# Kernel tuning notes

Hardware: AMD Instinct MI355X
Metric: run time of the kernel (lower is better)

The kernel has to match this reference:

```python
import jax, jax.numpy as jnp
import numpy as np

TOP_K = 8
NUM_EXPERTS = 64
TEMPERATURE = 1.0
ALPHA = 0.01
EPS = 1e-20


def setup_inputs() -> dict:
    key = jax.random.key(0)
    k1, k2 = jax.random.split(key)
    hidden_states = jax.random.normal(k1, (4, 8192, 1024), dtype=jnp.float32)
    # kaiming_uniform-ish scale for the router weight
    bound = 1.0 / np.sqrt(1024.0)
    weight = jax.random.uniform(k2, (NUM_EXPERTS, 1024), dtype=jnp.float32,
                                minval=-bound, maxval=bound)
    return {"hidden_states": hidden_states, "weight": weight}


def reference(hidden_states, weight):
    bsz, seq_len, hidden_dim = hidden_states.shape
    flat = hidden_states.reshape(-1, hidden_dim)            # [N, H], N = bsz*seq_len
    logits = jnp.einsum('nh,eh->ne', flat, weight) / TEMPERATURE  # [N, E]
    scores = jax.nn.softmax(logits, axis=-1)                # [N, E]
    topk_weight, topk_idx = jax.lax.top_k(scores, TOP_K)    # [N, k] each
    # renormalize top-k probabilities
    topk_weight = topk_weight / (topk_weight.sum(axis=-1, keepdims=True) + EPS)
    # aux load-balancing loss (seq_aux=False branch), scores detached
    scores_aux = jax.lax.stop_gradient(scores)
    idx_flat = topk_idx.reshape(-1)                         # [N*k]
    ce = jnp.zeros((NUM_EXPERTS,), dtype=jnp.float32).at[idx_flat].add(1.0)
    ce = ce / idx_flat.shape[0]                             # mean of one-hot rows
    pi = scores_aux.mean(axis=0)                            # [E]
    fi = ce * NUM_EXPERTS
    aux_loss = (pi * fi).sum() * ALPHA
    return topk_idx, topk_weight, aux_loss
```

## Files before the change

### kernel.cpp

```cpp
#include <hip/hip_runtime.h>

#define H 1024
#define E 64
#define BT 64
#define THETA 2e-4f

typedef __attribute__((ext_vector_type(4))) float f4;
typedef __attribute__((ext_vector_type(16))) float f32x16;
typedef __bf16 bf16x8 __attribute__((ext_vector_type(8)));
typedef unsigned int u32;
typedef __attribute__((ext_vector_type(4))) u32 u32x4;

__device__ __forceinline__ u32 cvtpk_bf16(float a, float b) {
    u32 r;
    asm("v_cvt_pk_bf16_f32 %0, %1, %2" : "=v"(r) : "v"(a), "v"(b));
    return r;
}
__device__ __forceinline__ float asfloat(u32 u) { union { u32 u; float f; } c; c.u = u; return c.f; }

__device__ __forceinline__ void split8(f4 a, f4 b, u32x4& hi, u32x4& lo) {
    float x0[4] = {a.x, a.z, b.x, b.z};
    float x1[4] = {a.y, a.w, b.y, b.w};
    #pragma unroll
    for (int i = 0; i < 4; ++i) {
        u32 h = cvtpk_bf16(x0[i], x1[i]);
        float r0 = x0[i] - asfloat(h << 16);
        float r1 = x1[i] - asfloat(h & 0xFFFF0000u);
        hi[i] = h;
        lo[i] = cvtpk_bf16(r0, r1);
    }
}

__device__ __forceinline__ void async16(const void* g, void* l) {
    __builtin_amdgcn_global_load_lds(
        (const __attribute__((address_space(1))) unsigned int*)g,
        (__attribute__((address_space(3))) unsigned int*)l,
        16, 0, 0);
}

__global__ __launch_bounds__(512, 4)
void gate_main(const float* __restrict__ hs, const float* __restrict__ wt,
               float* __restrict__ out, float* __restrict__ pi_ws,
               float* __restrict__ ce_ws, unsigned int* __restrict__ risk_cnt,
               unsigned int* __restrict__ risk_list, unsigned int risk_cap,
               int n_tokens) {
    __shared__ float smem[16384];
    const int t = threadIdx.x;
    const int wave = t >> 6, lane = t & 63;
    const int tok_base = blockIdx.x * BT;
    char* sb = (char*)smem;

    const int srow = t >> 3;
    const int srcj = (t & 7) ^ (srow & 7);
    const float* gA = hs + (size_t)(tok_base + srow) * H + srcj * 4;
    const float* gB = wt + (size_t)srow * H + srcj * 4;
    const int sdest = wave << 10;

    const int lr = lane & 31, kh = lane >> 5;
    const int q4 = wave & 3, kh2 = wave >> 2;
    const int wrow = (q4 >> 1) * 32;
    const int wcol = (q4 & 1) * 32;
    const int arow = wrow + lr, brow = wcol + lr;
    const int s0 = kh2 * 4 + kh * 2;
    const int aoff = arow * 128 + ((s0 ^ (arow & 7)) << 4);
    const int boff = 8192 + brow * 128 + ((s0 ^ (brow & 7)) << 4);

    f32x16 acc0, acc1;
    #pragma unroll
    for (int i = 0; i < 16; ++i) { acc0[i] = 0.f; acc1[i] = 0.f; }

    auto stage = [&](int c) {
        char* bb = sb + (c & 3) * 16384;
        async16(gA + c * 32, bb + sdest);
        async16(gB + c * 32, bb + 8192 + sdest);
    };
    auto compute = [&](int c) {
        const char* cb = sb + (c & 3) * 16384;
        f4 a0 = *(const f4*)(cb + aoff);
        f4 a1 = *(const f4*)(cb + (aoff ^ 16));
        f4 b0 = *(const f4*)(cb + boff);
        f4 b1 = *(const f4*)(cb + (boff ^ 16));
        u32x4 ahp, alp, bhp, blp;
        split8(a0, a1, ahp, alp);
        split8(b0, b1, bhp, blp);
        const bf16x8 ah = __builtin_bit_cast(bf16x8, ahp);
        const bf16x8 al = __builtin_bit_cast(bf16x8, alp);
        const bf16x8 bh = __builtin_bit_cast(bf16x8, bhp);
        const bf16x8 bl = __builtin_bit_cast(bf16x8, blp);
        acc0 = __builtin_amdgcn_mfma_f32_32x32x16_bf16(ah, bh, acc0, 0, 0, 0);
        acc1 = __builtin_amdgcn_mfma_f32_32x32x16_bf16(ah, bl, acc1, 0, 0, 0);
        acc1 = __builtin_amdgcn_mfma_f32_32x32x16_bf16(al, bh, acc1, 0, 0, 0);
    };

    stage(0); stage(1); stage(2);
    for (int c = 0; c < 30; ++c) {
        asm volatile("s_waitcnt vmcnt(4)" ::: "memory");
        __builtin_amdgcn_s_barrier();
        __builtin_amdgcn_sched_barrier(0);
        if (c < 29) stage(c + 3);
        __builtin_amdgcn_sched_barrier(0);
        compute(c);
    }
    asm volatile("s_waitcnt vmcnt(2)" ::: "memory");
    __builtin_amdgcn_s_barrier();
    __builtin_amdgcn_sched_barrier(0);
    compute(30);
    asm volatile("s_waitcnt vmcnt(0)" ::: "memory");
    __builtin_amdgcn_s_barrier();
    __builtin_amdgcn_sched_barrier(0);
    compute(31);
    __syncthreads();

    float* S = smem;
    f4* S4 = (f4*)smem;
    float* P2    = smem + 4352;
    float* recip = smem + 8448;
    float* hist  = smem + 8512;
    float* pi7   = smem + 8576;

    {
        float vs[16];
        #pragma unroll
        for (int i = 0; i < 16; ++i) vs[i] = acc0[i] + acc1[i];
        if (kh2) {
            #pragma unroll
            for (int gq = 0; gq < 4; ++gq)
                #pragma unroll
                for (int qq = 0; qq < 4; ++qq)
                    P2[q4 * 1024 + (qq + gq * 8 + kh * 4) * 32 + lr] = vs[gq * 4 + qq];
        }
        if (t < 64) hist[t] = 0.f;
        __syncthreads();
        if (!kh2) {
            #pragma unroll
            for (int gq = 0; gq < 4; ++gq)
                #pragma unroll
                for (int qq = 0; qq < 4; ++qq) {
                    const int row = qq + gq * 8 + kh * 4;
                    S[(wrow + row) * 68 + wcol + lr] =
                        vs[gq * 4 + qq] + P2[q4 * 1024 + row * 32 + lr];
                }
        }
    }
    __syncthreads();

    if (t < 256) {
        const int tok = t >> 2, q = t & 3;
        f4 v[4];
        #pragma unroll
        for (int c2 = 0; c2 < 4; ++c2) v[c2] = S4[tok * 17 + q * 4 + c2];
        float m = v[0].x;
        #pragma unroll
        for (int c2 = 0; c2 < 4; ++c2)
            m = fmaxf(m, fmaxf(fmaxf(v[c2].x, v[c2].y), fmaxf(v[c2].z, v[c2].w)));
        m = fmaxf(m, __shfl_xor(m, 1, 64));
        m = fmaxf(m, __shfl_xor(m, 2, 64));
        float lsum = 0.f;
        #pragma unroll
        for (int c2 = 0; c2 < 4; ++c2) {
            v[c2].x = __expf(v[c2].x - m); v[c2].y = __expf(v[c2].y - m);
            v[c2].z = __expf(v[c2].z - m); v[c2].w = __expf(v[c2].w - m);
            lsum += (v[c2].x + v[c2].y) + (v[c2].z + v[c2].w);
        }
        #pragma unroll
        for (int c2 = 0; c2 < 4; ++c2) S4[tok * 17 + q * 4 + c2] = v[c2];
        lsum += __shfl_xor(lsum, 1, 64);
        lsum += __shfl_xor(lsum, 2, 64);
        if (q == 0) recip[tok] = 1.0f / lsum;
    }
    __syncthreads();

    const int selw = blockIdx.x & 7;
    if (wave == selw) {
        const int tok = lane;
        const int tok_g = tok_base + tok;
        float val[9]; int idx[9];
        #pragma unroll
        for (int r = 0; r < 9; ++r) { val[r] = -1.f; idx[r] = 0; }
        #pragma unroll
        for (int c2 = 0; c2 < 16; ++c2) {
            f4 v = S4[tok * 17 + c2];
            float e4[4] = {v.x, v.y, v.z, v.w};
            #pragma unroll
            for (int u = 0; u < 4; ++u) {
                float cv = e4[u]; int ci = c2 * 4 + u;
                #pragma unroll
                for (int r = 0; r < 9; ++r) {
                    const bool g = cv > val[r];
                    const float tv = val[r]; const int ti = idx[r];
                    val[r] = g ? cv : tv;  idx[r] = g ? ci : ti;
                    cv = g ? tv : cv;      ci = g ? ti : ci;
                }
            }
        }
        const float s8 = ((val[0] + val[1]) + (val[2] + val[3]))
                       + ((val[4] + val[5]) + (val[6] + val[7]));
        const float wsum = s8 + 1e-20f;
        f4* out4 = (f4*)out;
        f4 o;
        o.x = (float)idx[0]; o.y = (float)idx[1]; o.z = (float)idx[2]; o.w = (float)idx[3];
        out4[(size_t)tok_g * 2] = o;
        o.x = (float)idx[4]; o.y = (float)idx[5]; o.z = (float)idx[6]; o.w = (float)idx[7];
        out4[(size_t)tok_g * 2 + 1] = o;
        const size_t wb = (size_t)n_tokens * 2;
        o.x = val[0] / wsum; o.y = val[1] / wsum; o.z = val[2] / wsum; o.w = val[3] / wsum;
        out4[wb + (size_t)tok_g * 2] = o;
        o.x = val[4] / wsum; o.y = val[5] / wsum; o.z = val[6] / wsum; o.w = val[7] / wsum;
        out4[wb + (size_t)tok_g * 2 + 1] = o;
        #pragma unroll
        for (int r = 0; r < 8; ++r) atomicAdd(&hist[idx[r]], 1.0f);
        float ming = 1e30f;
        #pragma unroll
        for (int r = 0; r < 8; ++r)
            ming = fminf(ming, (val[r] - val[r + 1]) / fmaxf(val[r], 1e-30f));
        if (ming < THETA) {
            unsigned int pos = atomicAdd(risk_cnt, 1u);
            if (pos < risk_cap) risk_list[pos] = (unsigned int)tok_g;
        }
    } else {
        const int sev = ((wave - selw) & 7) - 1;
        const int e = lane;
        const int t0 = sev * 9;
        const int t1 = (sev == 6) ? 64 : (t0 + 9);
        float part = 0.f;
        for (int tok = t0; tok < t1; ++tok)
            part = fmaf(S[tok * 68 + e], recip[tok], part);
        pi7[sev * 64 + e] = part;
    }
    __syncthreads();
    const int rep = (blockIdx.x & 7) << 6;
    if (t < 64) {
        const float p = ((pi7[t] + pi7[64 + t]) + (pi7[128 + t] + pi7[192 + t]))
                      + ((pi7[256 + t] + pi7[320 + t]) + pi7[384 + t]);
        atomicAdd(&pi_ws[rep + t], p);
    } else if (t < 128) {
        atomicAdd(&ce_ws[rep + (t - 64)], hist[t - 64]);
    }
}

__global__ __launch_bounds__(256)
void gate_fixup(const float* __restrict__ hs, const float* __restrict__ wt,
                float* __restrict__ out, const unsigned int* __restrict__ risk_cnt,
                const unsigned int* __restrict__ risk_list, unsigned int risk_cap,
                int n_tokens, const float* __restrict__ pi_ws,
                const float* __restrict__ ce_ws) {
    __shared__ float hrow[H];
    __shared__ double red[256];
    const int t = threadIdx.x;

    if (blockIdx.x == 0 && t < 64) {
        double pi = 0.0, ce = 0.0;
        #pragma unroll
        for (int rp = 0; rp < 8; ++rp) {
            pi += (double)pi_ws[rp * 64 + t];
            ce += (double)ce_ws[rp * 64 + t];
        }
        pi /= (double)n_tokens;
        ce /= ((double)n_tokens * 8.0);
        double term = pi * ce * 64.0;
        #pragma unroll
        for (int off = 32; off > 0; off >>= 1) term += __shfl_xor(term, off, 64);
        if (t == 0) out[(size_t)n_tokens * 16] = (float)(term * 0.01);
    }

    unsigned int cnt = *risk_cnt;
    if (cnt > risk_cap) cnt = risk_cap;

    for (unsigned int u = blockIdx.x; u < cnt; u += gridDim.x) {
        const int tok = (int)risk_list[u];
        ((float4*)hrow)[t] = ((const float4*)(hs + (size_t)tok * H))[t];
        __syncthreads();

        const int e = t >> 2, sl = t & 3;
        const float4* wp = (const float4*)wt + (size_t)e * 256;
        const float4* hp = (const float4*)hrow;
        double acc = 0.0;
        #pragma unroll 8
        for (int k4 = 0; k4 < 64; ++k4) {
            float4 wv = wp[k4 * 4 + sl];
            float4 hv = hp[k4 * 4 + sl];
            acc = fma((double)wv.x, (double)hv.x, acc);
            acc = fma((double)wv.y, (double)hv.y, acc);
            acc = fma((double)wv.z, (double)hv.z, acc);
            acc = fma((double)wv.w, (double)hv.w, acc);
        }
        red[t] = acc;
        __syncthreads();

        if (t < 64) {
            const int lane = t;
            double lg = red[t * 4] + red[t * 4 + 1] + red[t * 4 + 2] + red[t * 4 + 3];
            double m = lg;
            #pragma unroll
            for (int off = 32; off > 0; off >>= 1) {
                double o = __shfl_xor(m, off, 64);
                m = (o > m) ? o : m;
            }
            const double p = exp(lg - m);
            double v = lg, psum = 0.0, mypv = 0.0;
            int myidx = 0;
            for (int r = 0; r < 8; ++r) {
                double bv = v; int bi = lane;
                #pragma unroll
                for (int off = 32; off > 0; off >>= 1) {
                    double ov = __shfl_xor(bv, off, 64);
                    int    oi = __shfl_xor(bi, off, 64);
                    if (ov > bv || (ov == bv && oi < bi)) { bv = ov; bi = oi; }
                }
                double pw = __shfl(p, bi, 64);
                psum += pw;
                if (lane == r) { myidx = bi; mypv = pw; }
                if (lane == bi) v = -1e300;
            }
            const double wsum = psum + 1e-20;
            if (lane < 8) {
                out[(size_t)tok * 8 + lane] = (float)myidx;
                out[(size_t)n_tokens * 8 + (size_t)tok * 8 + lane] = (float)(mypv / wsum);
            }
        }
        __syncthreads();
    }
}

extern "C" void kernel_launch(void* const* d_in, const int* in_sizes, int n_in,
                              void* d_out, int out_size, void* d_ws, size_t ws_size,
                              hipStream_t stream) {
    const float* hs = (const float*)d_in[0];
    const float* wt = (const float*)d_in[1];
    float* out = (float*)d_out;
    const int n_tokens = in_sizes[0] / H;

    float* pi_ws = (float*)d_ws;
    float* ce_ws = (float*)((char*)d_ws + 2048);
    unsigned int* risk_cnt  = (unsigned int*)((char*)d_ws + 4096);
    unsigned int* risk_list = (unsigned int*)((char*)d_ws + 4608);
    unsigned int risk_cap = (unsigned int)((ws_size > 4608 ? (ws_size - 4608) : 0) / 4);
    if (risk_cap > (unsigned int)n_tokens) risk_cap = (unsigned int)n_tokens;

    size_t zbytes = ws_size < 4608 ? ws_size : 4608;
    hipMemsetAsync(d_ws, 0, zbytes, stream);

    gate_main<<<n_tokens / BT, 512, 0, stream>>>(hs, wt, out, pi_ws, ce_ws,
                                                 risk_cnt, risk_list, risk_cap, n_tokens);
    gate_fixup<<<256, 256, 0, stream>>>(hs, wt, out, risk_cnt, risk_list, risk_cap,
                                        n_tokens, pi_ws, ce_ws);
}
```

Measured before the change: 238.5 us.

## Halve token tile to 32 with 256-thread blocks, 3-stage ring and fragment prefetch

```diff
diff --git a/kernel.cpp b/kernel.cpp
--- a/kernel.cpp
+++ b/kernel.cpp
@@ -2,8 +2,8 @@
 
 #define H 1024
 #define E 64
-#define BT 64
-#define THETA 2e-4f
+#define BT 32
+#define THETA 1e-4f
 
 typedef __attribute__((ext_vector_type(4))) float f4;
 typedef __attribute__((ext_vector_type(16))) float f32x16;
@@ -38,85 +38,99 @@
         16, 0, 0);
 }
 
-__global__ __launch_bounds__(512, 4)
+__global__ __launch_bounds__(256, 4)
 void gate_main(const float* __restrict__ hs, const float* __restrict__ wt,
                float* __restrict__ out, float* __restrict__ pi_ws,
                float* __restrict__ ce_ws, unsigned int* __restrict__ risk_cnt,
                unsigned int* __restrict__ risk_list, unsigned int risk_cap,
                int n_tokens) {
-    __shared__ float smem[16384];
+    __shared__ float smem[9216];
     const int t = threadIdx.x;
     const int wave = t >> 6, lane = t & 63;
     const int tok_base = blockIdx.x * BT;
     char* sb = (char*)smem;
 
-    const int srow = t >> 3;
-    const int srcj = (t & 7) ^ (srow & 7);
-    const float* gA = hs + (size_t)(tok_base + srow) * H + srcj * 4;
-    const float* gB = wt + (size_t)srow * H + srcj * 4;
-    const int sdest = wave << 10;
+    const int arow_s  = t >> 3;
+    const int aslot_s = (t & 7) ^ (arow_s & 7);
+    const float* gA  = hs + (size_t)(tok_base + arow_s) * H + aslot_s * 4;
+    const int brow1  = t >> 3;
+    const int bslot1 = (t & 7) ^ (brow1 & 7);
+    const float* gB1 = wt + (size_t)brow1 * H + bslot1 * 4;
+    const int brow2  = (t + 256) >> 3;
+    const int bslot2 = (t & 7) ^ (brow2 & 7);
+    const float* gB2 = wt + (size_t)brow2 * H + bslot2 * 4;
+    const int dA  = t * 16;
+    const int dB1 = 4096 + t * 16;
+    const int dB2 = 8192 + t * 16;
 
     const int lr = lane & 31, kh = lane >> 5;
-    const int q4 = wave & 3, kh2 = wave >> 2;
-    const int wrow = (q4 >> 1) * 32;
-    const int wcol = (q4 & 1) * 32;
-    const int arow = wrow + lr, brow = wcol + lr;
+    const int e2 = wave & 1, kh2 = wave >> 1;
     const int s0 = kh2 * 4 + kh * 2;
-    const int aoff = arow * 128 + ((s0 ^ (arow & 7)) << 4);
-    const int boff = 8192 + brow * 128 + ((s0 ^ (brow & 7)) << 4);
+    const int arow = lr;
+    const int brow = e2 * 32 + lr;
+    const int aoff0 = arow * 128 + ((s0 ^ (arow & 7)) << 4);
+    const int aoff1 = arow * 128 + (((s0 + 1) ^ (arow & 7)) << 4);
+    const int boff0 = 4096 + brow * 128 + ((s0 ^ (brow & 7)) << 4);
+    const int boff1 = 4096 + brow * 128 + (((s0 + 1) ^ (brow & 7)) << 4);
 
     f32x16 acc0, acc1;
     #pragma unroll
     for (int i = 0; i < 16; ++i) { acc0[i] = 0.f; acc1[i] = 0.f; }
 
     auto stage = [&](int c) {
-        char* bb = sb + (c & 3) * 16384;
-        async16(gA + c * 32, bb + sdest);
-        async16(gB + c * 32, bb + 8192 + sdest);
+        char* bb = sb + (c % 3) * 12288;
+        const int co = c * 32;
+        async16(gA  + co, bb + dA);
+        async16(gB1 + co, bb + dB1);
+        async16(gB2 + co, bb + dB2);
     };
-    auto compute = [&](int c) {
-        const char* cb = sb + (c & 3) * 16384;
-        f4 a0 = *(const f4*)(cb + aoff);
-        f4 a1 = *(const f4*)(cb + (aoff ^ 16));
-        f4 b0 = *(const f4*)(cb + boff);
-        f4 b1 = *(const f4*)(cb + (boff ^ 16));
+
+    f4 fa0[2], fa1[2], fb0[2], fb1[2];
+    auto fragread = [&](int c, int p) {
+        const char* cb = sb + (c % 3) * 12288;
+        fa0[p] = *(const f4*)(cb + aoff0);
+        fa1[p] = *(const f4*)(cb + aoff1);
+        fb0[p] = *(const f4*)(cb + boff0);
+        fb1[p] = *(const f4*)(cb + boff1);
+    };
+    auto computeF = [&](int p) {
         u32x4 ahp, alp, bhp, blp;
-        split8(a0, a1, ahp, alp);
-        split8(b0, b1, bhp, blp);
+        split8(fa0[p], fa1[p], ahp, alp);
+        split8(fb0[p], fb1[p], bhp, blp);
         const bf16x8 ah = __builtin_bit_cast(bf16x8, ahp);
         const bf16x8 al = __builtin_bit_cast(bf16x8, alp);
         const bf16x8 bh = __builtin_bit_cast(bf16x8, bhp);
         const bf16x8 bl = __builtin_bit_cast(bf16x8, blp);
+        __builtin_amdgcn_s_setprio(1);
         acc0 = __builtin_amdgcn_mfma_f32_32x32x16_bf16(ah, bh, acc0, 0, 0, 0);
         acc1 = __builtin_amdgcn_mfma_f32_32x32x16_bf16(ah, bl, acc1, 0, 0, 0);
         acc1 = __builtin_amdgcn_mfma_f32_32x32x16_bf16(al, bh, acc1, 0, 0, 0);
+        __builtin_amdgcn_s_setprio(0);
     };
 
-    stage(0); stage(1); stage(2);
-    for (int c = 0; c < 30; ++c) {
-        asm volatile("s_waitcnt vmcnt(4)" ::: "memory");
-        __builtin_amdgcn_s_barrier();
-        __builtin_amdgcn_sched_barrier(0);
-        if (c < 29) stage(c + 3);
-        __builtin_amdgcn_sched_barrier(0);
-        compute(c);
-    }
-    asm volatile("s_waitcnt vmcnt(2)" ::: "memory");
+    stage(0); stage(1);
+    asm volatile("s_waitcnt vmcnt(3)" ::: "memory");
     __builtin_amdgcn_s_barrier();
-    __builtin_amdgcn_sched_barrier(0);
-    compute(30);
-    asm volatile("s_waitcnt vmcnt(0)" ::: "memory");
-    __builtin_amdgcn_s_barrier();
-    __builtin_amdgcn_sched_barrier(0);
-    compute(31);
+    fragread(0, 0);
+    #pragma unroll 2
+    for (int c = 0; c < 32; ++c) {
+        if (c + 2 < 32) stage(c + 2);
+        if (c + 1 < 32) {
+            if (c + 1 < 31) { asm volatile("s_waitcnt vmcnt(3)" ::: "memory"); }
+            else            { asm volatile("s_waitcnt vmcnt(0)" ::: "memory"); }
+            __builtin_amdgcn_s_barrier();
+            fragread(c + 1, (c + 1) & 1);
+        }
+        computeF(c & 1);
+    }
     __syncthreads();
 
     float* S = smem;
     f4* S4 = (f4*)smem;
-    float* P2    = smem + 4352;
-    float* recip = smem + 8448;
-    float* hist  = smem + 8512;
-    float* pi7   = smem + 8576;
+    float* P2    = smem + 2176;
+    float* recip = smem + 4224;
+    float* hist  = smem + 4256;
+    float* pi3   = smem + 4320;
 
     {
         float vs[16];
@@ -127,7 +141,7 @@
             for (int gq = 0; gq < 4; ++gq)
                 #pragma unroll
                 for (int qq = 0; qq < 4; ++qq)
-                    P2[q4 * 1024 + (qq + gq * 8 + kh * 4) * 32 + lr] = vs[gq * 4 + qq];
+                    P2[e2 * 1024 + (qq + gq * 8 + kh * 4) * 32 + lr] = vs[gq * 4 + qq];
         }
         if (t < 64) hist[t] = 0.f;
         __syncthreads();
@@ -137,14 +151,14 @@
                 #pragma unroll
                 for (int qq = 0; qq < 4; ++qq) {
                     const int row = qq + gq * 8 + kh * 4;
-                    S[(wrow + row) * 68 + wcol + lr] =
-                        vs[gq * 4 + qq] + P2[q4 * 1024 + row * 32 + lr];
+                    S[row * 68 + e2 * 32 + lr] =
+                        vs[gq * 4 + qq] + P2[e2 * 1024 + row * 32 + lr];
                 }
         }
     }
     __syncthreads();
 
-    if (t < 256) {
+    if (t < 128) {
         const int tok = t >> 2, q = t & 3;
         f4 v[4];
         #pragma unroll
@@ -170,69 +184,69 @@
     }
     __syncthreads();
 
-    const int selw = blockIdx.x & 7;
+    const int selw = blockIdx.x & 3;
     if (wave == selw) {
-        const int tok = lane;
-        const int tok_g = tok_base + tok;
-        float val[9]; int idx[9];
-        #pragma unroll
-        for (int r = 0; r < 9; ++r) { val[r] = -1.f; idx[r] = 0; }
-        #pragma unroll
-        for (int c2 = 0; c2 < 16; ++c2) {
-            f4 v = S4[tok * 17 + c2];
-            float e4[4] = {v.x, v.y, v.z, v.w};
-            #pragma unroll
-            for (int u = 0; u < 4; ++u) {
-                float cv = e4[u]; int ci = c2 * 4 + u;
+        if (lane < 32) {
+            const int tok = lane;
+            const int tok_g = tok_base + tok;
+            float val[9]; int idx[9];
+            #pragma unroll
+            for (int r = 0; r < 9; ++r) { val[r] = -1.f; idx[r] = 0; }
+            #pragma unroll
+            for (int c2 = 0; c2 < 16; ++c2) {
+                f4 v = S4[tok * 17 + c2];
+                float e4[4] = {v.x, v.y, v.z, v.w};
                 #pragma unroll
-                for (int r = 0; r < 9; ++r) {
-                    const bool g = cv > val[r];
-                    const float tv = val[r]; const int ti = idx[r];
-                    val[r] = g ? cv : tv;  idx[r] = g ? ci : ti;
-                    cv = g ? tv : cv;      ci = g ? ti : ci;
+                for (int u = 0; u < 4; ++u) {
+                    float cv = e4[u]; int ci = c2 * 4 + u;
+                    #pragma unroll
+                    for (int r = 0; r < 9; ++r) {
+                        const bool g = cv > val[r];
+                        const float tv = val[r]; const int ti = idx[r];
+                        val[r] = g ? cv : tv;  idx[r] = g ? ci : ti;
+                        cv = g ? tv : cv;      ci = g ? ti : ci;
+                    }
                 }
             }
-        }
-        const float s8 = ((val[0] + val[1]) + (val[2] + val[3]))
-                       + ((val[4] + val[5]) + (val[6] + val[7]));
-        const float wsum = s8 + 1e-20f;
-        f4* out4 = (f4*)out;
-        f4 o;
-        o.x = (float)idx[0]; o.y = (float)idx[1]; o.z = (float)idx[2]; o.w = (float)idx[3];
-        out4[(size_t)tok_g * 2] = o;
-        o.x = (float)idx[4]; o.y = (float)idx[5]; o.z = (float)idx[6]; o.w = (float)idx[7];
-        out4[(size_t)tok_g * 2 + 1] = o;
-        const size_t wb = (size_t)n_tokens * 2;
-        o.x = val[0] / wsum; o.y = val[1] / wsum; o.z = val[2] / wsum; o.w = val[3] / wsum;
-        out4[wb + (size_t)tok_g * 2] = o;
-        o.x = val[4] / wsum; o.y = val[5] / wsum; o.z = val[6] / wsum; o.w = val[7] / wsum;
-        out4[wb + (size_t)tok_g * 2 + 1] = o;
-        #pragma unroll
-        for (int r = 0; r < 8; ++r) atomicAdd(&hist[idx[r]], 1.0f);
-        float ming = 1e30f;
-        #pragma unroll
-        for (int r = 0; r < 8; ++r)
-            ming = fminf(ming, (val[r] - val[r + 1]) / fmaxf(val[r], 1e-30f));
-        if (ming < THETA) {
-            unsigned int pos = atomicAdd(risk_cnt, 1u);
-            if (pos < risk_cap) risk_list[pos] = (unsigned int)tok_g;
+            const float s8 = ((val[0] + val[1]) + (val[2] + val[3]))
+                           + ((val[4] + val[5]) + (val[6] + val[7]));
+            const float wsum = s8 + 1e-20f;
+            f4* out4 = (f4*)out;
+            f4 o;
+            o.x = (float)idx[0]; o.y = (float)idx[1]; o.z = (float)idx[2]; o.w = (float)idx[3];
+            out4[(size_t)tok_g * 2] = o;
+            o.x = (float)idx[4]; o.y = (float)idx[5]; o.z = (float)idx[6]; o.w = (float)idx[7];
+            out4[(size_t)tok_g * 2 + 1] = o;
+            const size_t wb = (size_t)n_tokens * 2;
+            o.x = val[0] / wsum; o.y = val[1] / wsum; o.z = val[2] / wsum; o.w = val[3] / wsum;
+            out4[wb + (size_t)tok_g * 2] = o;
+            o.x = val[4] / wsum; o.y = val[5] / wsum; o.z = val[6] / wsum; o.w = val[7] / wsum;
+            out4[wb + (size_t)tok_g * 2 + 1] = o;
+            #pragma unroll
+            for (int r = 0; r < 8; ++r) atomicAdd(&hist[idx[r]], 1.0f);
+            float ming = 1e30f;
+            #pragma unroll
+            for (int r = 0; r < 8; ++r)
+                ming = fminf(ming, (val[r] - val[r + 1]) / fmaxf(val[r], 1e-30f));
+            if (ming < THETA) {
+                unsigned int pos = atomicAdd(risk_cnt, 1u);
+                if (pos < risk_cap) risk_list[pos] = (unsigned int)tok_g;
+            }
         }
     } else {
-        const int sev = ((wave - selw) & 7) - 1;
+        const int third = ((wave - selw) & 3) - 1;
         const int e = lane;
-        const int t0 = sev * 9;
-        const int t1 = (sev == 6) ? 64 : (t0 + 9);
+        const int t0 = third * 11;
+        const int t1 = (third == 2) ? 32 : (t0 + 11);
         float part = 0.f;
         for (int tok = t0; tok < t1; ++tok)
             part = fmaf(S[tok * 68 + e], recip[tok], part);
-        pi7[sev * 64 + e] = part;
+        pi3[third * 64 + e] = part;
     }
     __syncthreads();
     const int rep = (blockIdx.x & 7) << 6;
     if (t < 64) {
-        const float p = ((pi7[t] + pi7[64 + t]) + (pi7[128 + t] + pi7[192 + t]))
-                      + ((pi7[256 + t] + pi7[320 + t]) + pi7[384 + t]);
-        atomicAdd(&pi_ws[rep + t], p);
+        atomicAdd(&pi_ws[rep + t], pi3[t] + pi3[64 + t] + pi3[128 + t]);
     } else if (t < 128) {
         atomicAdd(&ce_ws[rep + (t - 64)], hist[t - 64]);
     }
@@ -340,7 +354,7 @@
     size_t zbytes = ws_size < 4608 ? ws_size : 4608;
     hipMemsetAsync(d_ws, 0, zbytes, stream);
 
-    gate_main<<<n_tokens / BT, 512, 0, stream>>>(hs, wt, out, pi_ws, ce_ws,
+    gate_main<<<n_tokens / BT, 256, 0, stream>>>(hs, wt, out, pi_ws, ce_ws,
                                                  risk_cnt, risk_list, risk_cap, n_tokens);
     gate_fixup<<<256, 256, 0, stream>>>(hs, wt, out, risk_cnt, risk_list, risk_cap,
                                         n_tokens, pi_ws, ce_ws);
```

New measurement: 237.4 us. No clear change (-0.5%).

## Double token tile to 128 with 1024 threads, load router weights directly to registers

Applied to the files above, without the earlier changes.

```diff
diff --git a/kernel.cpp b/kernel.cpp
--- a/kernel.cpp
+++ b/kernel.cpp
@@ -2,8 +2,8 @@
 
 #define H 1024
 #define E 64
-#define BT 64
-#define THETA 2e-4f
+#define BT 128
+#define THETA 1e-4f
 
 typedef __attribute__((ext_vector_type(4))) float f4;
 typedef __attribute__((ext_vector_type(16))) float f32x16;
@@ -38,13 +38,13 @@
         16, 0, 0);
 }
 
-__global__ __launch_bounds__(512, 4)
+__global__ __launch_bounds__(1024, 4)
 void gate_main(const float* __restrict__ hs, const float* __restrict__ wt,
                float* __restrict__ out, float* __restrict__ pi_ws,
                float* __restrict__ ce_ws, unsigned int* __restrict__ risk_cnt,
                unsigned int* __restrict__ risk_list, unsigned int risk_cap,
                int n_tokens) {
-    __shared__ float smem[16384];
+    __shared__ float smem[12288];
     const int t = threadIdx.x;
     const int wave = t >> 6, lane = t & 63;
     const int tok_base = blockIdx.x * BT;
@@ -53,36 +53,53 @@
     const int srow = t >> 3;
     const int srcj = (t & 7) ^ (srow & 7);
     const float* gA = hs + (size_t)(tok_base + srow) * H + srcj * 4;
-    const float* gB = wt + (size_t)srow * H + srcj * 4;
     const int sdest = wave << 10;
 
     const int lr = lane & 31, kh = lane >> 5;
-    const int q4 = wave & 3, kh2 = wave >> 2;
-    const int wrow = (q4 >> 1) * 32;
-    const int wcol = (q4 & 1) * 32;
-    const int arow = wrow + lr, brow = wcol + lr;
+    const int tq = wave & 3, ch = (wave >> 2) & 1, kh2 = wave >> 3;
+    const int wrow = tq * 32, wcol = ch * 32;
+    const int arow = wrow + lr;
     const int s0 = kh2 * 4 + kh * 2;
-    const int aoff = arow * 128 + ((s0 ^ (arow & 7)) << 4);
-    const int boff = 8192 + brow * 128 + ((s0 ^ (brow & 7)) << 4);
+    const int aoff0 = arow * 128 + (((s0    ) ^ (arow & 7)) << 4);
+    const int aoff1 = arow * 128 + (((s0 + 1) ^ (arow & 7)) << 4);
+    const float* gB = wt + (size_t)(wcol + lr) * H + kh2 * 16 + kh * 8;
 
     f32x16 acc0, acc1;
     #pragma unroll
     for (int i = 0; i < 16; ++i) { acc0[i] = 0.f; acc1[i] = 0.f; }
 
     auto stage = [&](int c) {
-        char* bb = sb + (c & 3) * 16384;
+        char* bb = sb + (c % 3) * 16384;
         async16(gA + c * 32, bb + sdest);
-        async16(gB + c * 32, bb + 8192 + sdest);
     };
-    auto compute = [&](int c) {
-        const char* cb = sb + (c & 3) * 16384;
-        f4 a0 = *(const f4*)(cb + aoff);
-        f4 a1 = *(const f4*)(cb + (aoff ^ 16));
-        f4 b0 = *(const f4*)(cb + boff);
-        f4 b1 = *(const f4*)(cb + (boff ^ 16));
+
+    f4 b0a, b1a, b0b, b1b;
+
+    stage(0); stage(1);
+    b0a = *(const f4*)(gB);
+    b1a = *(const f4*)(gB + 4);
+
+    #pragma unroll 2
+    for (int c = 0; c < 32; ++c) {
+        __builtin_amdgcn_sched_barrier(0);
+        if (c < 31) { asm volatile("s_waitcnt vmcnt(3)" ::: "memory"); }
+        else        { asm volatile("s_waitcnt vmcnt(2)" ::: "memory"); }
+        __builtin_amdgcn_s_barrier();
+        __builtin_amdgcn_sched_barrier(0);
+        if (c + 1 < 32) {
+            const float* p = gB + (c + 1) * 32;
+            if ((c & 1) == 0) { b0b = *(const f4*)p; b1b = *(const f4*)(p + 4); }
+            else              { b0a = *(const f4*)p; b1a = *(const f4*)(p + 4); }
+        }
+        if (c + 2 < 32) stage(c + 2);
+        __builtin_amdgcn_sched_barrier(0);
+        const char* cb = sb + (c % 3) * 16384;
+        f4 a0 = *(const f4*)(cb + aoff0);
+        f4 a1 = *(const f4*)(cb + aoff1);
         u32x4 ahp, alp, bhp, blp;
         split8(a0, a1, ahp, alp);
-        split8(b0, b1, bhp, blp);
+        if ((c & 1) == 0) split8(b0a, b1a, bhp, blp);
+        else              split8(b0b, b1b, bhp, blp);
         const bf16x8 ah = __builtin_bit_cast(bf16x8, ahp);
         const bf16x8 al = __builtin_bit_cast(bf16x8, alp);
         const bf16x8 bh = __builtin_bit_cast(bf16x8, bhp);
@@ -90,61 +107,43 @@
         acc0 = __builtin_amdgcn_mfma_f32_32x32x16_bf16(ah, bh, acc0, 0, 0, 0);
         acc1 = __builtin_amdgcn_mfma_f32_32x32x16_bf16(ah, bl, acc1, 0, 0, 0);
         acc1 = __builtin_amdgcn_mfma_f32_32x32x16_bf16(al, bh, acc1, 0, 0, 0);
-    };
-
-    stage(0); stage(1); stage(2);
-    for (int c = 0; c < 30; ++c) {
-        asm volatile("s_waitcnt vmcnt(4)" ::: "memory");
-        __builtin_amdgcn_s_barrier();
-        __builtin_amdgcn_sched_barrier(0);
-        if (c < 29) stage(c + 3);
-        __builtin_amdgcn_sched_barrier(0);
-        compute(c);
-    }
-    asm volatile("s_waitcnt vmcnt(2)" ::: "memory");
-    __builtin_amdgcn_s_barrier();
-    __builtin_amdgcn_sched_barrier(0);
-    compute(30);
-    asm volatile("s_waitcnt vmcnt(0)" ::: "memory");
-    __builtin_amdgcn_s_barrier();
-    __builtin_amdgcn_sched_barrier(0);
-    compute(31);
+    }
     __syncthreads();
 
     float* S = smem;
     f4* S4 = (f4*)smem;
-    float* P2    = smem + 4352;
-    float* recip = smem + 8448;
-    float* hist  = smem + 8512;
-    float* pi7   = smem + 8576;
+    float* recip = smem + 8704;
+    float* hist  = smem + 8832;
+    float* pi14  = smem + 8896;
 
     {
         float vs[16];
         #pragma unroll
         for (int i = 0; i < 16; ++i) vs[i] = acc0[i] + acc1[i];
-        if (kh2) {
-            #pragma unroll
-            for (int gq = 0; gq < 4; ++gq)
-                #pragma unroll
-                for (int qq = 0; qq < 4; ++qq)
-                    P2[q4 * 1024 + (qq + gq * 8 + kh * 4) * 32 + lr] = vs[gq * 4 + qq];
-        }
-        if (t < 64) hist[t] = 0.f;
-        __syncthreads();
         if (!kh2) {
             #pragma unroll
             for (int gq = 0; gq < 4; ++gq)
                 #pragma unroll
                 for (int qq = 0; qq < 4; ++qq) {
                     const int row = qq + gq * 8 + kh * 4;
-                    S[(wrow + row) * 68 + wcol + lr] =
-                        vs[gq * 4 + qq] + P2[q4 * 1024 + row * 32 + lr];
+                    S[(wrow + row) * 68 + wcol + lr] = vs[gq * 4 + qq];
                 }
         }
+        if (t < 64) hist[t] = 0.f;
+        __syncthreads();
+        if (kh2) {
+            #pragma unroll
+            for (int gq = 0; gq < 4; ++gq)
+                #pragma unroll
+                for (int qq = 0; qq < 4; ++qq) {
+                    const int row = qq + gq * 8 + kh * 4;
+                    atomicAdd(&S[(wrow + row) * 68 + wcol + lr], vs[gq * 4 + qq]);
+                }
+        }
     }
     __syncthreads();
 
-    if (t < 256) {
+    if (t < 512) {
         const int tok = t >> 2, q = t & 3;
         f4 v[4];
         #pragma unroll
@@ -170,9 +169,8 @@
     }
     __syncthreads();
 
-    const int selw = blockIdx.x & 7;
-    if (wave == selw) {
-        const int tok = lane;
+    if (wave >= 14) {
+        const int tok = (wave - 14) * 64 + lane;
         const int tok_g = tok_base + tok;
         float val[9]; int idx[9];
         #pragma unroll
@@ -218,20 +216,20 @@
             if (pos < risk_cap) risk_list[pos] = (unsigned int)tok_g;
         }
     } else {
-        const int sev = ((wave - selw) & 7) - 1;
         const int e = lane;
-        const int t0 = sev * 9;
-        const int t1 = (sev == 6) ? 64 : (t0 + 9);
+        const int t0 = (wave * 128) / 14;
+        const int t1 = ((wave + 1) * 128) / 14;
         float part = 0.f;
         for (int tok = t0; tok < t1; ++tok)
             part = fmaf(S[tok * 68 + e], recip[tok], part);
-        pi7[sev * 64 + e] = part;
+        pi14[wave * 64 + e] = part;
     }
     __syncthreads();
     const int rep = (blockIdx.x & 7) << 6;
     if (t < 64) {
-        const float p = ((pi7[t] + pi7[64 + t]) + (pi7[128 + t] + pi7[192 + t]))
-                      + ((pi7[256 + t] + pi7[320 + t]) + pi7[384 + t]);
+        float p = 0.f;
+        #pragma unroll
+        for (int i = 0; i < 14; ++i) p += pi14[i * 64 + t];
         atomicAdd(&pi_ws[rep + t], p);
     } else if (t < 128) {
         atomicAdd(&ce_ws[rep + (t - 64)], hist[t - 64]);
@@ -340,8 +338,8 @@
     size_t zbytes = ws_size < 4608 ? ws_size : 4608;
     hipMemsetAsync(d_ws, 0, zbytes, stream);
 
-    gate_main<<<n_tokens / BT, 512, 0, stream>>>(hs, wt, out, pi_ws, ce_ws,
-                                                 risk_cnt, risk_list, risk_cap, n_tokens);
+    gate_main<<<n_tokens / BT, 1024, 0, stream>>>(hs, wt, out, pi_ws, ce_ws,
+                                                  risk_cnt, risk_list, risk_cap, n_tokens);
     gate_fixup<<<256, 256, 0, stream>>>(hs, wt, out, risk_cnt, risk_list, risk_cap,
                                         n_tokens, pi_ws, ce_ws);
 }
```

New measurement: 251.6 us. 1.05x slower.

## Load router weights directly into registers and halve LDS staging buffers

Applied to the files above, without the earlier changes.

```diff
diff --git a/kernel.cpp b/kernel.cpp
--- a/kernel.cpp
+++ b/kernel.cpp
@@ -3,7 +3,7 @@
 #define H 1024
 #define E 64
 #define BT 64
-#define THETA 2e-4f
+#define THETA 1e-4f
 
 typedef __attribute__((ext_vector_type(4))) float f4;
 typedef __attribute__((ext_vector_type(16))) float f32x16;
@@ -44,7 +44,7 @@
                float* __restrict__ ce_ws, unsigned int* __restrict__ risk_cnt,
                unsigned int* __restrict__ risk_list, unsigned int risk_cap,
                int n_tokens) {
-    __shared__ float smem[16384];
+    __shared__ float smem[8192];
     const int t = threadIdx.x;
     const int wave = t >> 6, lane = t & 63;
     const int tok_base = blockIdx.x * BT;
@@ -53,36 +53,33 @@
     const int srow = t >> 3;
     const int srcj = (t & 7) ^ (srow & 7);
     const float* gA = hs + (size_t)(tok_base + srow) * H + srcj * 4;
-    const float* gB = wt + (size_t)srow * H + srcj * 4;
     const int sdest = wave << 10;
 
     const int lr = lane & 31, kh = lane >> 5;
     const int q4 = wave & 3, kh2 = wave >> 2;
     const int wrow = (q4 >> 1) * 32;
     const int wcol = (q4 & 1) * 32;
-    const int arow = wrow + lr, brow = wcol + lr;
+    const int arow = wrow + lr;
     const int s0 = kh2 * 4 + kh * 2;
-    const int aoff = arow * 128 + ((s0 ^ (arow & 7)) << 4);
-    const int boff = 8192 + brow * 128 + ((s0 ^ (brow & 7)) << 4);
+    const int aoff0 = arow * 128 + (((s0    ) ^ (arow & 7)) << 4);
+    const int aoff1 = arow * 128 + (((s0 + 1) ^ (arow & 7)) << 4);
+    const float* gBb = wt + (size_t)(wcol + lr) * H + s0 * 4;
 
     f32x16 acc0, acc1;
     #pragma unroll
     for (int i = 0; i < 16; ++i) { acc0[i] = 0.f; acc1[i] = 0.f; }
 
     auto stage = [&](int c) {
-        char* bb = sb + (c & 3) * 16384;
+        char* bb = sb + (c & 3) * 8192;
         async16(gA + c * 32, bb + sdest);
-        async16(gB + c * 32, bb + 8192 + sdest);
     };
-    auto compute = [&](int c) {
-        const char* cb = sb + (c & 3) * 16384;
-        f4 a0 = *(const f4*)(cb + aoff);
-        f4 a1 = *(const f4*)(cb + (aoff ^ 16));
-        f4 b0 = *(const f4*)(cb + boff);
-        f4 b1 = *(const f4*)(cb + (boff ^ 16));
+    auto compute = [&](int c, f4 bb0, f4 bb1) {
+        const char* cb = sb + (c & 3) * 8192;
+        f4 a0 = *(const f4*)(cb + aoff0);
+        f4 a1 = *(const f4*)(cb + aoff1);
         u32x4 ahp, alp, bhp, blp;
         split8(a0, a1, ahp, alp);
-        split8(b0, b1, bhp, blp);
+        split8(bb0, bb1, bhp, blp);
         const bf16x8 ah = __builtin_bit_cast(bf16x8, ahp);
         const bf16x8 al = __builtin_bit_cast(bf16x8, alp);
         const bf16x8 bh = __builtin_bit_cast(bf16x8, bhp);
@@ -92,53 +89,82 @@
         acc1 = __builtin_amdgcn_mfma_f32_32x32x16_bf16(al, bh, acc1, 0, 0, 0);
     };
 
+    f4 b0a = *(const f4*)(gBb);
+    f4 b1a = *(const f4*)(gBb + 4);
+    f4 b0b, b1b;
     stage(0); stage(1); stage(2);
-    for (int c = 0; c < 30; ++c) {
-        asm volatile("s_waitcnt vmcnt(4)" ::: "memory");
+
+    asm volatile("s_waitcnt vmcnt(2)" ::: "memory");
+    __builtin_amdgcn_s_barrier();
+    __builtin_amdgcn_sched_barrier(0);
+    b0b = *(const f4*)(gBb + 32); b1b = *(const f4*)(gBb + 36);
+    stage(3);
+    __builtin_amdgcn_sched_barrier(0);
+    compute(0, b0a, b1a);
+
+    asm volatile("s_waitcnt vmcnt(4)" ::: "memory");
+    __builtin_amdgcn_s_barrier();
+    __builtin_amdgcn_sched_barrier(0);
+    b0a = *(const f4*)(gBb + 64); b1a = *(const f4*)(gBb + 68);
+    stage(4);
+    __builtin_amdgcn_sched_barrier(0);
+    compute(1, b0b, b1b);
+
+    #pragma unroll 2
+    for (int c = 2; c < 30; ++c) {
+        asm volatile("s_waitcnt vmcnt(6)" ::: "memory");
         __builtin_amdgcn_s_barrier();
         __builtin_amdgcn_sched_barrier(0);
+        const float* p = gBb + (c + 1) * 32;
+        if ((c & 1) == 0) { b0b = *(const f4*)p; b1b = *(const f4*)(p + 4); }
+        else              { b0a = *(const f4*)p; b1a = *(const f4*)(p + 4); }
         if (c < 29) stage(c + 3);
         __builtin_amdgcn_sched_barrier(0);
-        compute(c);
-    }
-    asm volatile("s_waitcnt vmcnt(2)" ::: "memory");
+        if ((c & 1) == 0) compute(c, b0a, b1a);
+        else              compute(c, b0b, b1b);
+    }
+
+    asm volatile("s_waitcnt vmcnt(5)" ::: "memory");
     __builtin_amdgcn_s_barrier();
     __builtin_amdgcn_sched_barrier(0);
-    compute(30);
-    asm volatile("s_waitcnt vmcnt(0)" ::: "memory");
+    b0b = *(const f4*)(gBb + 31 * 32); b1b = *(const f4*)(gBb + 31 * 32 + 4);
+    __builtin_amdgcn_sched_barrier(0);
+    compute(30, b0a, b1a);
+
+    asm volatile("s_waitcnt vmcnt(4)" ::: "memory");
     __builtin_amdgcn_s_barrier();
     __builtin_amdgcn_sched_barrier(0);
-    compute(31);
+    compute(31, b0b, b1b);
     __syncthreads();
 
     float* S = smem;
     f4* S4 = (f4*)smem;
-    float* P2    = smem + 4352;
-    float* recip = smem + 8448;
-    float* hist  = smem + 8512;
-    float* pi7   = smem + 8576;
+    float* recip = smem + 4352;
+    float* hist  = smem + 4416;
+    float* pi7   = smem + 4480;
 
     {
         float vs[16];
         #pragma unroll
         for (int i = 0; i < 16; ++i) vs[i] = acc0[i] + acc1[i];
-        if (kh2) {
-            #pragma unroll
-            for (int gq = 0; gq < 4; ++gq)
-                #pragma unroll
-                for (int qq = 0; qq < 4; ++qq)
-                    P2[q4 * 1024 + (qq + gq * 8 + kh * 4) * 32 + lr] = vs[gq * 4 + qq];
-        }
-        if (t < 64) hist[t] = 0.f;
-        __syncthreads();
         if (!kh2) {
             #pragma unroll
             for (int gq = 0; gq < 4; ++gq)
                 #pragma unroll
                 for (int qq = 0; qq < 4; ++qq) {
                     const int row = qq + gq * 8 + kh * 4;
-                    S[(wrow + row) * 68 + wcol + lr] =
-                        vs[gq * 4 + qq] + P2[q4 * 1024 + row * 32 + lr];
+                    S[(wrow + row) * 68 + wcol + lr] = vs[gq * 4 + qq];
+                }
+        }
+        if (t < 64) hist[t] = 0.f;
+        __syncthreads();
+        if (kh2) {
+            #pragma unroll
+            for (int gq = 0; gq < 4; ++gq)
+                #pragma unroll
+                for (int qq = 0; qq < 4; ++qq) {
+                    const int row = qq + gq * 8 + kh * 4;
+                    atomicAdd(&S[(wrow + row) * 68 + wcol + lr], vs[gq * 4 + qq]);
                 }
         }
     }
```

After: 242.5 us. No clear change (+1.7%).
